# Kernel tuning notes

Measured on AMD Instinct MI355X. Metric: run time of the kernel, lower is better.

Reference implementation:

```python
import jax, jax.numpy as jnp
import numpy as np

B, S, E, H = 4, 2048, 1024, 16
D = E // H
LR_MULT = 100.0
EPS = 1e-5

def setup_inputs() -> dict:
    key = jax.random.key(0)
    ks = jax.random.split(key, 4)
    x = jax.random.normal(ks[0], (B, S, E), dtype=jnp.float32)
    # nn.MultiheadAttention in_proj_weight [3E,E], out_proj.weight [E,E] (bias=False)
    W_qkv = jax.random.normal(ks[1], (3 * E, E), dtype=jnp.float32) * (1.0 / np.sqrt(E))
    W_o = jax.random.normal(ks[2], (E, E), dtype=jnp.float32) * (1.0 / np.sqrt(E))
    ln_w = jnp.ones((E,), dtype=jnp.float32)
    scaler = jnp.asarray(1.0 / LR_MULT, dtype=jnp.float32)
    return {"x": x, "W_qkv": W_qkv, "W_o": W_o, "ln_w": ln_w, "scaler": scaler}

def _layernorm(x, w):
    mu = jnp.mean(x, axis=-1, keepdims=True)
    var = jnp.mean(jnp.square(x - mu), axis=-1, keepdims=True)
    return (x - mu) * jax.lax.rsqrt(var + EPS) * w

def reference(x, W_qkv, W_o, ln_w, scaler):
    resid = x
    xn = _layernorm(x, ln_w)
    qkv = jnp.einsum('bse,fe->bsf', xn, W_qkv)  # [B,S,3E]
    q, k, v = jnp.split(qkv, 3, axis=-1)
    q = q.reshape(B, S, H, D)
    k = k.reshape(B, S, H, D)
    v = v.reshape(B, S, H, D)
    scores = jnp.einsum('bihd,bjhd->bhij', q, k) / jnp.sqrt(jnp.asarray(D, x.dtype))
    # linear_encoding_base[i,j] = j - i; bias = softplus(100*scaler)*(j-i) where j<=i else -inf
    i_idx = jnp.arange(S)
    rel = (i_idx[None, :] - i_idx[:, None]).astype(x.dtype)  # j - i
    causal = i_idx[None, :] <= i_idx[:, None]                # tril: j <= i
    slope = jax.nn.softplus(LR_MULT * scaler)
    bias = jnp.where(causal, slope * rel, -jnp.inf)          # [S,S]
    att = jax.nn.softmax(scores + bias[None, None, :, :], axis=-1)
    out = jnp.einsum('bhij,bjhd->bihd', att, v).reshape(B, S, E)
    out = jnp.einsum('bse,fe->bsf', out, W_o)
    return out + resid
```

## Files before the change

kernel.cpp:

```cpp
#include <hip/hip_runtime.h>

typedef unsigned short u16;
typedef unsigned int u32;
typedef __bf16 bf16x8 __attribute__((ext_vector_type(8)));
typedef float f32x4 __attribute__((ext_vector_type(4)));

#define B_ 4
#define S_ 2048
#define E_ 1024
#define H_ 16
#define D_ 64

__device__ __forceinline__ u16 f2bf(float f) {
  u32 u = __float_as_uint(f);
  u32 r = u + 0x7fffu + ((u >> 16) & 1u);
  return (u16)(r >> 16);
}

__device__ __forceinline__ void gload16(const u16* g, u16* l) {
  __builtin_amdgcn_global_load_lds((const __attribute__((address_space(1))) void*)g,
                                   (__attribute__((address_space(3))) void*)l, 16, 0, 0);
}

__global__ __launch_bounds__(256) void ln_kernel(const float* __restrict__ x,
                                                 const float* __restrict__ w,
                                                 u16* __restrict__ xn) {
  const int lane = threadIdx.x & 63;
  const int wv = threadIdx.x >> 6;
  const int row = blockIdx.x * 4 + wv;
  const float4* xr = (const float4*)(x + (size_t)row * E_);
  float4 vv[4];
  float s = 0.f, sq = 0.f;
#pragma unroll
  for (int i = 0; i < 4; ++i) {
    vv[i] = xr[lane + i * 64];
    s += vv[i].x + vv[i].y + vv[i].z + vv[i].w;
    sq += vv[i].x * vv[i].x + vv[i].y * vv[i].y + vv[i].z * vv[i].z + vv[i].w * vv[i].w;
  }
#pragma unroll
  for (int off = 1; off < 64; off <<= 1) {
    s += __shfl_xor(s, off);
    sq += __shfl_xor(sq, off);
  }
  const float mu = s * (1.f / E_);
  const float rs = rsqrtf(sq * (1.f / E_) - mu * mu + 1e-5f);
  u16* xo = xn + (size_t)row * E_;
  const float4* wr = (const float4*)w;
#pragma unroll
  for (int i = 0; i < 4; ++i) {
    float4 w4 = wr[lane + i * 64];
    ushort4 o;
    o.x = f2bf((vv[i].x - mu) * rs * w4.x);
    o.y = f2bf((vv[i].y - mu) * rs * w4.y);
    o.z = f2bf((vv[i].z - mu) * rs * w4.z);
    o.w = f2bf((vv[i].w - mu) * rs * w4.w);
    ((ushort4*)xo)[lane + i * 64] = o;
  }
}

__global__ __launch_bounds__(256) void cvt_kernel(const float* __restrict__ src,
                                                  u16* __restrict__ dst) {
  const int i = blockIdx.x * 256 + threadIdx.x;
  float4 v = ((const float4*)src)[i];
  ushort4 o;
  o.x = f2bf(v.x);
  o.y = f2bf(v.y);
  o.z = f2bf(v.z);
  o.w = f2bf(v.w);
  ((ushort4*)dst)[i] = o;
}

template <int EPI>
__global__ __launch_bounds__(256, 2) void gemm_bt(const u16* __restrict__ A,
                                                  const u16* __restrict__ Bw,
                                                  const int K,
                                                  u16* __restrict__ qo, u16* __restrict__ ko,
                                                  u16* __restrict__ vo,
                                                  const float* __restrict__ xres,
                                                  float* __restrict__ outp) {
  __shared__ u16 lds[2][2][128 * 64];
  const int t = threadIdx.x;
  const int lane = t & 63, wv = t >> 6;
  const int wm = wv >> 1, wn = wv & 1;
  const int m0 = blockIdx.y * 128, n0 = blockIdx.x * 128;
  const int r16 = lane & 15, g4 = lane >> 4;

  const f32x4 fzero = {0.f, 0.f, 0.f, 0.f};
  f32x4 acc[4][4];
#pragma unroll
  for (int i = 0; i < 4; ++i)
#pragma unroll
    for (int j = 0; j < 4; ++j) acc[i][j] = fzero;

  const int srow8 = lane >> 3;
  const int scol = (lane & 7) * 8;

  auto stage = [&](int bu, int kt) {
#pragma unroll
    for (int i = 0; i < 4; ++i) {
      const int c = wv * 4 + i;
      const int row = c * 8 + srow8;
      gload16(A + (size_t)(m0 + row) * K + kt + scol, &lds[bu][0][c * 512]);
      gload16(Bw + (size_t)(n0 + row) * K + kt + scol, &lds[bu][1][c * 512]);
    }
  };

  auto compute = [&](int bu) {
    const u16* As = lds[bu][0];
    const u16* Bs = lds[bu][1];
    bf16x8 af[4][2], bfr[4][2];
#pragma unroll
    for (int mi = 0; mi < 4; ++mi)
#pragma unroll
      for (int kc = 0; kc < 2; ++kc)
        af[mi][kc] = *(const bf16x8*)&As[(wm * 64 + mi * 16 + r16) * 64 + kc * 32 + g4 * 8];
#pragma unroll
    for (int ni = 0; ni < 4; ++ni)
#pragma unroll
      for (int kc = 0; kc < 2; ++kc)
        bfr[ni][kc] = *(const bf16x8*)&Bs[(wn * 64 + ni * 16 + r16) * 64 + kc * 32 + g4 * 8];
#pragma unroll
    for (int mi = 0; mi < 4; ++mi)
#pragma unroll
      for (int ni = 0; ni < 4; ++ni)
#pragma unroll
        for (int kc = 0; kc < 2; ++kc)
          acc[mi][ni] = __builtin_amdgcn_mfma_f32_16x16x32_bf16(af[mi][kc], bfr[ni][kc],
                                                                acc[mi][ni], 0, 0, 0);
  };

  stage(0, 0);
  __syncthreads();
  int cur = 0;
  for (int kt = 64; kt < K; kt += 64) {
    stage(cur ^ 1, kt);
    compute(cur);
    __syncthreads();
    cur ^= 1;
  }
  compute(cur);

  if constexpr (EPI == 0) {
    const int which = n0 >> 10;
    u16* dst = which == 0 ? qo : (which == 1 ? ko : vo);
#pragma unroll
    for (int mi = 0; mi < 4; ++mi)
#pragma unroll
      for (int e = 0; e < 4; ++e) {
        const int gr = m0 + wm * 64 + mi * 16 + g4 * 4 + e;
        const int bb = gr >> 11, ss = gr & 2047;
#pragma unroll
        for (int ni = 0; ni < 4; ++ni) {
          const int gc = n0 + wn * 64 + ni * 16 + r16;
          const int hh = (gc >> 6) & 15;
          const int dd = gc & 63;
          dst[(((size_t)bb * H_ + hh) * S_ + ss) * D_ + dd] = f2bf(acc[mi][ni][e]);
        }
      }
  } else {
#pragma unroll
    for (int mi = 0; mi < 4; ++mi)
#pragma unroll
      for (int e = 0; e < 4; ++e) {
        const int gr = m0 + wm * 64 + mi * 16 + g4 * 4 + e;
#pragma unroll
        for (int ni = 0; ni < 4; ++ni) {
          const int gc = n0 + wn * 64 + ni * 16 + r16;
          const size_t idx = (size_t)gr * 1024 + gc;
          outp[idx] = acc[mi][ni][e] + xres[idx];
        }
      }
  }
}

__global__ __launch_bounds__(256) void attn_kernel(const u16* __restrict__ q,
                                                   const u16* __restrict__ k,
                                                   const u16* __restrict__ v,
                                                   const float* __restrict__ scaler_p,
                                                   u16* __restrict__ ao) {
  __shared__ u16 Qs[64 * 72];
  __shared__ u16 Ks[64 * 72];
  __shared__ u16 Vt[64 * 72];
  __shared__ u16 Ps[4 * 16 * 72];
  const int t = threadIdx.x;
  const int lane = t & 63, wv = t >> 6;
  const int r16 = lane & 15, g4 = lane >> 4;
  const int it = blockIdx.x;
  const int bh = blockIdx.y;
  const int bb = bh >> 4, hh = bh & 15;
  const size_t base = (size_t)bh * (S_ * D_);

  const float tt = 100.f * scaler_p[0];
  const float slope = (tt > 20.f) ? tt : log1pf(expf(tt));
  const float L2E = 1.4426950408889634f;
  const float qs_l2e = 0.125f * L2E;
  const float sl_l2e = slope * L2E;
  int nb = (int)ceilf(80.f / (slope * 64.f));
  if (nb < 1) nb = 1;
  int jt0 = it - nb;
  if (jt0 < 0) jt0 = 0;

  {
    const int r = t >> 2, c = (t & 3) << 4;
    const u16* gp = q + base + (size_t)(it * 64 + r) * D_ + c;
    uint4 a0 = ((const uint4*)gp)[0];
    uint4 a1 = ((const uint4*)gp)[1];
    *(uint4*)&Qs[r * 72 + c] = a0;
    *(uint4*)&Qs[r * 72 + c + 8] = a1;
  }

  float mrun[4] = {-3e38f, -3e38f, -3e38f, -3e38f};
  float lrun[4] = {0.f, 0.f, 0.f, 0.f};
  const f32x4 fzero = {0.f, 0.f, 0.f, 0.f};
  f32x4 oacc[4];
#pragma unroll
  for (int i = 0; i < 4; ++i) oacc[i] = fzero;

  bf16x8 qa[2];
  bool qloaded = false;

  for (int jt = jt0; jt <= it; ++jt) {
    {
      const int r = t >> 2, c = (t & 3) << 4;
      const u16* kg = k + base + (size_t)(jt * 64 + r) * D_ + c;
      uint4 k0 = ((const uint4*)kg)[0];
      uint4 k1 = ((const uint4*)kg)[1];
      *(uint4*)&Ks[r * 72 + c] = k0;
      *(uint4*)&Ks[r * 72 + c + 8] = k1;
      const u16* vg = v + base + (size_t)(jt * 64 + r) * D_ + c;
      union { uint4 u; u16 s[8]; } v0, v1;
      v0.u = ((const uint4*)vg)[0];
      v1.u = ((const uint4*)vg)[1];
#pragma unroll
      for (int j = 0; j < 8; ++j) {
        Vt[(c + j) * 72 + r] = v0.s[j];
        Vt[(c + 8 + j) * 72 + r] = v1.s[j];
      }
    }
    __syncthreads();
    if (!qloaded) {
      qloaded = true;
#pragma unroll
      for (int kc = 0; kc < 2; ++kc)
        qa[kc] = *(const bf16x8*)&Qs[(wv * 16 + r16) * 72 + kc * 32 + g4 * 8];
    }
    f32x4 sfr[4];
#pragma unroll
    for (int nt = 0; nt < 4; ++nt) {
      sfr[nt] = fzero;
#pragma unroll
      for (int kc = 0; kc < 2; ++kc) {
        bf16x8 kb = *(const bf16x8*)&Ks[(nt * 16 + r16) * 72 + kc * 32 + g4 * 8];
        sfr[nt] = __builtin_amdgcn_mfma_f32_16x16x32_bf16(qa[kc], kb, sfr[nt], 0, 0, 0);
      }
    }
    const bool diag = (jt == it);
    const float jb = (float)((jt - it) * 64);
    float pm[4] = {-3e38f, -3e38f, -3e38f, -3e38f};
#pragma unroll
    for (int nt = 0; nt < 4; ++nt) {
      const int jl = nt * 16 + r16;
#pragma unroll
      for (int e = 0; e < 4; ++e) {
        const int il = wv * 16 + g4 * 4 + e;
        float sc = sfr[nt][e] * qs_l2e + sl_l2e * (jb + (float)(jl - il));
        if (diag && jl > il) sc = -3e38f;
        sfr[nt][e] = sc;
        pm[e] = fmaxf(pm[e], sc);
      }
    }
#pragma unroll
    for (int e = 0; e < 4; ++e) {
#pragma unroll
      for (int off = 1; off < 16; off <<= 1) pm[e] = fmaxf(pm[e], __shfl_xor(pm[e], off));
    }
    u16* Psw = Ps + wv * (16 * 72);
    float psum[4] = {0.f, 0.f, 0.f, 0.f};
#pragma unroll
    for (int e = 0; e < 4; ++e) {
      const float mn = fmaxf(mrun[e], pm[e]);
      const float rsc = exp2f(mrun[e] - mn);
      mrun[e] = mn;
      lrun[e] *= rsc;
#pragma unroll
      for (int nt = 0; nt < 4; ++nt) oacc[nt][e] *= rsc;
    }
#pragma unroll
    for (int nt = 0; nt < 4; ++nt)
#pragma unroll
      for (int e = 0; e < 4; ++e) {
        const float p = exp2f(sfr[nt][e] - mrun[e]);
        psum[e] += p;
        Psw[(g4 * 4 + e) * 72 + nt * 16 + r16] = f2bf(p);
      }
#pragma unroll
    for (int e = 0; e < 4; ++e) {
#pragma unroll
      for (int off = 1; off < 16; off <<= 1) psum[e] += __shfl_xor(psum[e], off);
      lrun[e] += psum[e];
    }
    bf16x8 pa[2];
#pragma unroll
    for (int jk = 0; jk < 2; ++jk)
      pa[jk] = *(const bf16x8*)&Psw[r16 * 72 + jk * 32 + g4 * 8];
#pragma unroll
    for (int nt = 0; nt < 4; ++nt)
#pragma unroll
      for (int jk = 0; jk < 2; ++jk) {
        bf16x8 vb = *(const bf16x8*)&Vt[(nt * 16 + r16) * 72 + jk * 32 + g4 * 8];
        oacc[nt] = __builtin_amdgcn_mfma_f32_16x16x32_bf16(pa[jk], vb, oacc[nt], 0, 0, 0);
      }
    __syncthreads();
  }
#pragma unroll
  for (int e = 0; e < 4; ++e) {
    const float inv = 1.f / lrun[e];
    const int row = it * 64 + wv * 16 + g4 * 4 + e;
#pragma unroll
    for (int nt = 0; nt < 4; ++nt) {
      const int col = hh * 64 + nt * 16 + r16;
      ao[((size_t)bb * S_ + row) * E_ + col] = f2bf(oacc[nt][e] * inv);
    }
  }
}

extern "C" void kernel_launch(void* const* d_in, const int* in_sizes, int n_in,
                              void* d_out, int out_size, void* d_ws, size_t ws_size,
                              hipStream_t stream) {
  const float* x = (const float*)d_in[0];
  const float* Wqkv = (const float*)d_in[1];
  const float* Wo = (const float*)d_in[2];
  const float* lnw = (const float*)d_in[3];
  const float* scaler = (const float*)d_in[4];
  float* out = (float*)d_out;
  char* ws = (char*)d_ws;

  u16* xn = (u16*)(ws + 0);
  u16* q = (u16*)(ws + 16777216);
  u16* kk = (u16*)(ws + 33554432);
  u16* vv = (u16*)(ws + 50331648);
  u16* ao = (u16*)(ws + 67108864);
  u16* wqkvb = (u16*)(ws + 83886080);
  u16* wob = (u16*)(ws + 90177536);

  ln_kernel<<<2048, 256, 0, stream>>>(x, lnw, xn);
  cvt_kernel<<<3072, 256, 0, stream>>>(Wqkv, wqkvb);
  cvt_kernel<<<1024, 256, 0, stream>>>(Wo, wob);
  gemm_bt<0><<<dim3(24, 64), 256, 0, stream>>>(xn, wqkvb, 1024, q, kk, vv, nullptr, nullptr);
  attn_kernel<<<dim3(32, 64), 256, 0, stream>>>(q, kk, vv, scaler, ao);
  gemm_bt<1><<<dim3(8, 64), 256, 0, stream>>>(ao, wob, 1024, nullptr, nullptr, nullptr, x, out);
}
```

Measured before the change: 141.5 us.

## Replace QKV GEMM with 256x256-tile 8-wave pipelined kernel

Adds a dedicated QKV projection kernel with 256x256 tiles, 512 threads and 8 waves. Each k-step is split into four phases that interleave global-to-LDS loads with MFMA work, using explicit waitcnt, barriers, setprio and an XOR-swizzled LDS layout. The larger tiles raise data reuse per load, and the phasing is meant to hide memory latency and LDS bank conflicts. The cost is 128KB of LDS per block and heavy register use, and the grid shrinks to 384 blocks, which may leave the GPU partly occupied.

```diff
diff --git a/kernel.cpp b/kernel.cpp
--- a/kernel.cpp
+++ b/kernel.cpp
@@ -70,14 +70,180 @@
   ((ushort4*)dst)[i] = o;
 }
 
-template <int EPI>
-__global__ __launch_bounds__(256, 2) void gemm_bt(const u16* __restrict__ A,
-                                                  const u16* __restrict__ Bw,
-                                                  const int K,
-                                                  u16* __restrict__ qo, u16* __restrict__ ko,
-                                                  u16* __restrict__ vo,
-                                                  const float* __restrict__ xres,
-                                                  float* __restrict__ outp) {
+__global__ __launch_bounds__(512, 2) void gemm8_qkv(const u16* __restrict__ A,
+                                                    const u16* __restrict__ Bw,
+                                                    u16* __restrict__ qo,
+                                                    u16* __restrict__ ko,
+                                                    u16* __restrict__ vo) {
+  constexpr int K = 1024;
+  constexpr int NT = K / 64;
+  __shared__ u16 lds[2][2][256 * 64];
+  const int t = threadIdx.x;
+  const int lane = t & 63, wv = t >> 6;
+  const int wm = wv >> 2, wn = wv & 3;
+  const int m0 = blockIdx.y * 256, n0 = blockIdx.x * 256;
+  const int r16 = lane & 15, g4 = lane >> 4;
+  const int l3 = lane >> 3, l7 = lane & 7;
+  const int colsrc = ((l7 ^ l3) * 8);
+
+  f32x4 acc[8][4] = {};
+  bf16x8 af[8][2];
+  bf16x8 bfr[2][2];
+
+  auto issue = [&](int ph, int buf, int kt) {
+#pragma unroll
+    for (int s = 0; s < 2; ++s) {
+      const int j = wv * 2 + s;
+      int c, m;
+      if (ph == 0)      { m = 0; c = j + (j & 8); }
+      else if (ph == 1) { m = 1; c = (j >> 2) * 8 + (j & 3); }
+      else if (ph == 2) { m = 0; c = 8 + j + (j & 8); }
+      else              { m = 1; c = (j >> 2) * 8 + 4 + (j & 3); }
+      const u16* src = (m == 0 ? A + (size_t)(m0 + c * 8 + l3) * K
+                               : Bw + (size_t)(n0 + c * 8 + l3) * K) + kt + colsrc;
+      gload16(src, &lds[buf][m][c * 512]);
+    }
+  };
+
+  auto loadA = [&](const u16* As, int half) {
+#pragma unroll
+    for (int i = 0; i < 4; ++i) {
+      const int mi = half * 4 + i;
+      const int r = wm * 128 + mi * 16 + r16;
+      const int sw = (r & 7) << 3;
+#pragma unroll
+      for (int kc = 0; kc < 2; ++kc)
+        af[mi][kc] = *(const bf16x8*)&As[r * 64 + ((kc * 32 + g4 * 8) ^ sw)];
+    }
+  };
+  auto loadB = [&](const u16* Bs, int pair) {
+#pragma unroll
+    for (int n2 = 0; n2 < 2; ++n2) {
+      const int r = wn * 64 + (pair * 2 + n2) * 16 + r16;
+      const int sw = (r & 7) << 3;
+#pragma unroll
+      for (int kc = 0; kc < 2; ++kc)
+        bfr[n2][kc] = *(const bf16x8*)&Bs[r * 64 + ((kc * 32 + g4 * 8) ^ sw)];
+    }
+  };
+  auto mmac = [&](int mhalf, int npair) {
+#pragma unroll
+    for (int i = 0; i < 4; ++i)
+#pragma unroll
+      for (int n2 = 0; n2 < 2; ++n2)
+#pragma unroll
+        for (int kc = 0; kc < 2; ++kc)
+          acc[mhalf * 4 + i][npair * 2 + n2] = __builtin_amdgcn_mfma_f32_16x16x32_bf16(
+              af[mhalf * 4 + i][kc], bfr[n2][kc], acc[mhalf * 4 + i][npair * 2 + n2], 0, 0, 0);
+  };
+
+  issue(0, 0, 0);
+  issue(1, 0, 0);
+  issue(2, 0, 0);
+  issue(3, 0, 0);
+  asm volatile("s_waitcnt vmcnt(0)" ::: "memory");
+  __builtin_amdgcn_s_barrier();
+
+  for (int kt2 = 0; kt2 < NT - 1; ++kt2) {
+    const int cur = kt2 & 1;
+    const u16* As = lds[cur][0];
+    const u16* Bs = lds[cur][1];
+    const int ktN = (kt2 + 1) * 64;
+    loadA(As, 0);
+    loadB(Bs, 0);
+    issue(0, cur ^ 1, ktN);
+    __builtin_amdgcn_s_barrier();
+    asm volatile("s_waitcnt lgkmcnt(0)" ::: "memory");
+    asm volatile("s_waitcnt vmcnt(6)" ::: "memory");
+    __builtin_amdgcn_sched_barrier(0);
+    __builtin_amdgcn_s_setprio(1);
+    mmac(0, 0);
+    __builtin_amdgcn_s_setprio(0);
+    __builtin_amdgcn_s_barrier();
+    loadA(As, 1);
+    issue(1, cur ^ 1, ktN);
+    __builtin_amdgcn_s_barrier();
+    asm volatile("s_waitcnt lgkmcnt(0)" ::: "memory");
+    asm volatile("s_waitcnt vmcnt(6)" ::: "memory");
+    __builtin_amdgcn_sched_barrier(0);
+    __builtin_amdgcn_s_setprio(1);
+    mmac(1, 0);
+    __builtin_amdgcn_s_setprio(0);
+    __builtin_amdgcn_s_barrier();
+    loadB(Bs, 1);
+    issue(2, cur ^ 1, ktN);
+    __builtin_amdgcn_s_barrier();
+    asm volatile("s_waitcnt lgkmcnt(0)" ::: "memory");
+    asm volatile("s_waitcnt vmcnt(6)" ::: "memory");
+    __builtin_amdgcn_sched_barrier(0);
+    __builtin_amdgcn_s_setprio(1);
+    mmac(1, 1);
+    __builtin_amdgcn_s_setprio(0);
+    __builtin_amdgcn_s_barrier();
+    issue(3, cur ^ 1, ktN);
+    __builtin_amdgcn_s_barrier();
+    __builtin_amdgcn_sched_barrier(0);
+    __builtin_amdgcn_s_setprio(1);
+    mmac(0, 1);
+    __builtin_amdgcn_s_setprio(0);
+    __builtin_amdgcn_s_barrier();
+  }
+  {
+    const int cur = (NT - 1) & 1;
+    const u16* As = lds[cur][0];
+    const u16* Bs = lds[cur][1];
+    loadA(As, 0);
+    loadB(Bs, 0);
+    __builtin_amdgcn_s_barrier();
+    asm volatile("s_waitcnt lgkmcnt(0)" ::: "memory");
+    asm volatile("s_waitcnt vmcnt(4)" ::: "memory");
+    __builtin_amdgcn_sched_barrier(0);
+    __builtin_amdgcn_s_setprio(1);
+    mmac(0, 0);
+    __builtin_amdgcn_s_setprio(0);
+    __builtin_amdgcn_s_barrier();
+    loadA(As, 1);
+    __builtin_amdgcn_s_barrier();
+    asm volatile("s_waitcnt lgkmcnt(0)" ::: "memory");
+    asm volatile("s_waitcnt vmcnt(2)" ::: "memory");
+    __builtin_amdgcn_sched_barrier(0);
+    __builtin_amdgcn_s_setprio(1);
+    mmac(1, 0);
+    __builtin_amdgcn_s_setprio(0);
+    __builtin_amdgcn_s_barrier();
+    loadB(Bs, 1);
+    asm volatile("s_waitcnt lgkmcnt(0)" ::: "memory");
+    asm volatile("s_waitcnt vmcnt(0)" ::: "memory");
+    __builtin_amdgcn_sched_barrier(0);
+    __builtin_amdgcn_s_setprio(1);
+    mmac(1, 1);
+    mmac(0, 1);
+    __builtin_amdgcn_s_setprio(0);
+  }
+
+  const int which = n0 >> 10;
+  u16* dst = which == 0 ? qo : (which == 1 ? ko : vo);
+#pragma unroll
+  for (int mi = 0; mi < 8; ++mi)
+#pragma unroll
+    for (int e = 0; e < 4; ++e) {
+      const int gr = m0 + wm * 128 + mi * 16 + g4 * 4 + e;
+      const int bb = gr >> 11, ss = gr & 2047;
+#pragma unroll
+      for (int ni = 0; ni < 4; ++ni) {
+        const int gc = n0 + wn * 64 + ni * 16 + r16;
+        const int hh = (gc >> 6) & 15;
+        const int dd = gc & 63;
+        dst[(((size_t)bb * H_ + hh) * S_ + ss) * D_ + dd] = f2bf(acc[mi][ni][e]);
+      }
+    }
+}
+
+__global__ __launch_bounds__(256, 2) void gemm_bt1(const u16* __restrict__ A,
+                                                   const u16* __restrict__ Bw,
+                                                   const int K,
+                                                   const float* __restrict__ xres,
+                                                   float* __restrict__ outp) {
   __shared__ u16 lds[2][2][128 * 64];
   const int t = threadIdx.x;
   const int lane = t & 63, wv = t >> 6;
@@ -140,37 +306,18 @@
   }
   compute(cur);
 
-  if constexpr (EPI == 0) {
-    const int which = n0 >> 10;
-    u16* dst = which == 0 ? qo : (which == 1 ? ko : vo);
-#pragma unroll
-    for (int mi = 0; mi < 4; ++mi)
-#pragma unroll
-      for (int e = 0; e < 4; ++e) {
-        const int gr = m0 + wm * 64 + mi * 16 + g4 * 4 + e;
-        const int bb = gr >> 11, ss = gr & 2047;
-#pragma unroll
-        for (int ni = 0; ni < 4; ++ni) {
-          const int gc = n0 + wn * 64 + ni * 16 + r16;
-          const int hh = (gc >> 6) & 15;
-          const int dd = gc & 63;
-          dst[(((size_t)bb * H_ + hh) * S_ + ss) * D_ + dd] = f2bf(acc[mi][ni][e]);
-        }
-      }
-  } else {
-#pragma unroll
-    for (int mi = 0; mi < 4; ++mi)
-#pragma unroll
-      for (int e = 0; e < 4; ++e) {
-        const int gr = m0 + wm * 64 + mi * 16 + g4 * 4 + e;
-#pragma unroll
-        for (int ni = 0; ni < 4; ++ni) {
-          const int gc = n0 + wn * 64 + ni * 16 + r16;
-          const size_t idx = (size_t)gr * 1024 + gc;
-          outp[idx] = acc[mi][ni][e] + xres[idx];
-        }
-      }
-  }
+#pragma unroll
+  for (int mi = 0; mi < 4; ++mi)
+#pragma unroll
+    for (int e = 0; e < 4; ++e) {
+      const int gr = m0 + wm * 64 + mi * 16 + g4 * 4 + e;
+#pragma unroll
+      for (int ni = 0; ni < 4; ++ni) {
+        const int gc = n0 + wn * 64 + ni * 16 + r16;
+        const size_t idx = (size_t)gr * 1024 + gc;
+        outp[idx] = acc[mi][ni][e] + xres[idx];
+      }
+    }
 }
 
 __global__ __launch_bounds__(256) void attn_kernel(const u16* __restrict__ q,
@@ -346,7 +493,7 @@
   ln_kernel<<<2048, 256, 0, stream>>>(x, lnw, xn);
   cvt_kernel<<<3072, 256, 0, stream>>>(Wqkv, wqkvb);
   cvt_kernel<<<1024, 256, 0, stream>>>(Wo, wob);
-  gemm_bt<0><<<dim3(24, 64), 256, 0, stream>>>(xn, wqkvb, 1024, q, kk, vv, nullptr, nullptr);
+  gemm8_qkv<<<dim3(12, 32), 512, 0, stream>>>(xn, wqkvb, q, kk, vv);
   attn_kernel<<<dim3(32, 64), 256, 0, stream>>>(q, kk, vv, scaler, ao);
-  gemm_bt<1><<<dim3(8, 64), 256, 0, stream>>>(ao, wob, 1024, nullptr, nullptr, nullptr, x, out);
-}
+  gemm_bt1<<<dim3(8, 64), 256, 0, stream>>>(ao, wob, 1024, x, out);
+}
```

After: 136.2 us. -3.7%, faster.
